# Optimization experiments

Measured on AMD Instinct MI355X. Metric: run time of the kernel, lower is better.

Reference implementation:

```python
import jax, jax.numpy as jnp
import numpy as np

B, D, H, W, Q = 16, 768, 64, 64, 128


def setup_inputs() -> dict:
    key = jax.random.key(0)
    ks = jax.random.split(key, 6)
    s = 0.02  # param init scale
    return {
        "visual_feat": jax.random.normal(ks[0], (B, D, H, W), jnp.float32),
        "text_feat": jax.random.normal(ks[1], (B, Q, D), jnp.float32),
        "Wq": jax.random.normal(ks[2], (D, D), jnp.float32) * s,
        "bq": jnp.zeros((D,), jnp.float32),
        "Wk": jax.random.normal(ks[3], (D, D), jnp.float32) * s,
        "bk": jnp.zeros((D,), jnp.float32),
        "Wv": jax.random.normal(ks[4], (D, D), jnp.float32) * s,
        "bv": jnp.zeros((D,), jnp.float32),
    }


def _entropy_weights(x):
    # x: [B, T, D] -> softmax over features, per-token entropy, softmax over tokens -> [B, T]
    p = jax.nn.softmax(x, axis=-1)
    ent = -jnp.sum(p * jnp.log(p + 1e-9), axis=-1)
    return jax.nn.softmax(ent, axis=-1)


def reference(visual_feat, text_feat, Wq, bq, Wk, bk, Wv, bv):
    b, d, h, w = visual_feat.shape
    vf = visual_feat.reshape(b, d, h * w).transpose(0, 2, 1)  # [B, N, D]
    ve = _entropy_weights(vf)          # [B, N]
    te = _entropy_weights(text_feat)   # [B, Q]
    q = vf @ Wq.T + bq                 # [B, N, D]
    k = text_feat @ Wk.T + bk          # [B, Q, D]
    v = text_feat @ Wv.T + bv          # [B, Q, D]
    attn = jnp.einsum('bnd,bqd->bnq', q, k) / jnp.sqrt(jnp.float32(d))
    attn = attn * (ve[:, :, None] * te[:, None, :])  # entropy outer-product modulation
    attn = jax.nn.softmax(attn, axis=-1)
    enhanced = jnp.einsum('bnq,bqd->bnd', attn, v)   # [B, N, D]
    return enhanced.transpose(0, 2, 1).reshape(b, d, h, w)
```

## Files before the change

kernel.cpp:

```cpp
#include <hip/hip_runtime.h>

#define B_ 16
#define D_ 768
#define N_ 4096
#define Q_ 128

typedef __attribute__((ext_vector_type(4))) float f32x4;
typedef __attribute__((ext_vector_type(8))) short short8;
typedef __attribute__((ext_vector_type(4))) short sv4;

__device__ __forceinline__ unsigned short f2bf(float f) {
  union { float f; unsigned u; } x; x.f = f;
  unsigned u = x.u;
  unsigned r = u + 0x7fffu + ((u >> 16) & 1u);
  return (unsigned short)(r >> 16);
}

__global__ __launch_bounds__(256) void prep_kernel(
    const float* __restrict__ Wv, const float* __restrict__ Wq,
    const float* __restrict__ Wk, const float* __restrict__ bq,
    const float* __restrict__ bk,
    unsigned short* __restrict__ Wvb, unsigned short* __restrict__ WqTb,
    unsigned short* __restrict__ WkTb,
    float* __restrict__ wkbq, float* __restrict__ bias2, float* __restrict__ bqbk) {
  __shared__ float tile[32][33];
  const int z = blockIdx.z;
  const int t = threadIdx.x;
  if (z == 0) {
    int i = (blockIdx.y * 24 + blockIdx.x) * 256 + t;
    float4 v = ((const float4*)Wv)[i];
    ushort4 o;
    o.x = f2bf(v.x); o.y = f2bf(v.y); o.z = f2bf(v.z); o.w = f2bf(v.w);
    ((ushort4*)Wvb)[i] = o;
  } else if (z <= 2) {
    const float* src = (z == 1) ? Wq : Wk;
    unsigned short* dst = (z == 1) ? WqTb : WkTb;
    int bx = blockIdx.x * 32, by = blockIdx.y * 32;
    int tx = t & 31, ty = t >> 5;
    #pragma unroll
    for (int i = 0; i < 32; i += 8)
      tile[ty + i][tx] = src[(size_t)(by + ty + i) * D_ + bx + tx];
    __syncthreads();
    #pragma unroll
    for (int i = 0; i < 32; i += 8)
      dst[(size_t)(bx + ty + i) * D_ + by + tx] = f2bf(tile[tx][ty + i]);
  } else {
    const int bx = blockIdx.x, by = blockIdx.y;
    if (by < 2) {
      if (bx >= 3) return;
      const float* M = by ? Wq : Wk;
      const float* vec = by ? bk : bq;
      float* outp = by ? bias2 : wkbq;
      const int col = bx * 256 + t;
      float s = 0.f;
      #pragma unroll 4
      for (int n = 0; n < D_; n++) s += M[(size_t)n * D_ + col] * vec[n];
      outp[col] = s;
    } else if (by == 2 && bx == 0) {
      float s = 0.f;
      for (int k = t; k < D_; k += 256) s += bq[k] * bk[k];
      #pragma unroll
      for (int off = 32; off; off >>= 1) s += __shfl_xor(s, off);
      __shared__ float red[4];
      if ((t & 63) == 0) red[t >> 6] = s;
      __syncthreads();
      if (t == 0) bqbk[0] = red[0] + red[1] + red[2] + red[3];
    }
  }
}

__global__ __launch_bounds__(256) void entropy_fused_kernel(
    const float* __restrict__ vis, float* __restrict__ ent_v,
    const float* __restrict__ text, unsigned short* __restrict__ textb,
    float* __restrict__ ent_t, const float* __restrict__ wkbq,
    const float* __restrict__ bqbk, float* __restrict__ skq) {
  __shared__ float ss[256], st[256];
  const int t = threadIdx.x;
  if (blockIdx.x < 1024) {
    int bb = blockIdx.x >> 6;
    int n0 = (blockIdx.x & 63) * 64;
    int tok = t & 63, slice = t >> 6;
    const float* base = vis + (size_t)bb * D_ * N_ + (size_t)slice * 192 * N_ + n0 + tok;
    float s = 0.f, tt = 0.f;
    #pragma unroll 4
    for (int d = 0; d < 192; d++) {
      float v = base[(size_t)d * N_];
      float e = __expf(v);
      s += e; tt += v * e;
    }
    ss[t] = s; st[t] = tt;
    __syncthreads();
    if (t < 64) {
      #pragma unroll
      for (int k = 1; k < 4; k++) { s += ss[t + 64 * k]; tt += st[t + 64 * k]; }
      ent_v[(size_t)bb * N_ + n0 + t] = __logf(s) - tt / s;
    }
  } else {
    int row = (blockIdx.x - 1024) * 4 + (t >> 6);
    int lane = t & 63;
    const float4* src = (const float4*)(text + (size_t)row * D_);
    const float4* w4p = (const float4*)wkbq;
    ushort4* dst = (ushort4*)(textb + (size_t)row * D_);
    float s = 0.f, tt = 0.f, s2 = 0.f;
    #pragma unroll
    for (int j = 0; j < 3; j++) {
      float4 v = src[lane + 64 * j];
      float4 w = w4p[lane + 64 * j];
      float e0 = __expf(v.x), e1 = __expf(v.y), e2 = __expf(v.z), e3 = __expf(v.w);
      s += (e0 + e1) + (e2 + e3);
      tt += v.x * e0 + v.y * e1;
      tt += v.z * e2 + v.w * e3;
      s2 += v.x * w.x + v.y * w.y + v.z * w.z + v.w * w.w;
      ushort4 o;
      o.x = f2bf(v.x); o.y = f2bf(v.y); o.z = f2bf(v.z); o.w = f2bf(v.w);
      dst[lane + 64 * j] = o;
    }
    #pragma unroll
    for (int off = 32; off; off >>= 1) {
      s += __shfl_xor(s, off);
      tt += __shfl_xor(tt, off);
      s2 += __shfl_xor(s2, off);
    }
    if (lane == 0) {
      ent_t[row] = __logf(s) - tt / s;
      skq[row] = s2 + bqbk[0];
    }
  }
}

__global__ __launch_bounds__(1024) void softmax_fused_kernel(
    const float* __restrict__ ent_v, float* __restrict__ vew,
    const float* __restrict__ ent_t, float* __restrict__ tew) {
  __shared__ float red[32];
  __shared__ float sv[128];
  const int b = blockIdx.x, t = threadIdx.x;
  if (b < 16) {
    const float* e = ent_v + (size_t)b * N_;
    float v[4];
    float m = -__builtin_inff();
    #pragma unroll
    for (int i = 0; i < 4; i++) { v[i] = e[t + 1024 * i]; m = fmaxf(m, v[i]); }
    #pragma unroll
    for (int off = 32; off; off >>= 1) m = fmaxf(m, __shfl_xor(m, off));
    int wv = t >> 6;
    if ((t & 63) == 0) red[wv] = m;
    __syncthreads();
    if (t < 16) {
      float x = red[t];
      #pragma unroll
      for (int off = 8; off; off >>= 1) x = fmaxf(x, __shfl_xor(x, off));
      red[t] = x;
    }
    __syncthreads();
    m = red[0];
    float ev[4];
    float s = 0.f;
    #pragma unroll
    for (int i = 0; i < 4; i++) { ev[i] = __expf(v[i] - m); s += ev[i]; }
    #pragma unroll
    for (int off = 32; off; off >>= 1) s += __shfl_xor(s, off);
    __syncthreads();
    if ((t & 63) == 0) red[wv] = s;
    __syncthreads();
    if (t < 16) {
      float x = red[t];
      #pragma unroll
      for (int off = 8; off; off >>= 1) x += __shfl_xor(x, off);
      red[t] = x;
    }
    __syncthreads();
    s = red[0];
    #pragma unroll
    for (int i = 0; i < 4; i++) vew[(size_t)b * N_ + t + 1024 * i] = ev[i] / s;
  } else {
    const int bb = b - 16;
    float v = 0.f;
    if (t < 128) { v = ent_t[bb * 128 + t]; sv[t] = v; }
    __syncthreads();
    if (t < 64) {
      float m = fmaxf(sv[t], sv[t + 64]);
      #pragma unroll
      for (int off = 32; off; off >>= 1) m = fmaxf(m, __shfl_xor(m, off));
      if (t == 0) red[0] = m;
    }
    __syncthreads();
    const float m = red[0];
    float e = 0.f;
    if (t < 128) { e = __expf(v - m); sv[t] = e; }
    __syncthreads();
    if (t < 64) {
      float s = sv[t] + sv[t + 64];
      #pragma unroll
      for (int off = 32; off; off >>= 1) s += __shfl_xor(s, off);
      if (t == 0) red[1] = s;
    }
    __syncthreads();
    if (t < 128) tew[bb * 128 + t] = e / red[1];
  }
}

__global__ __launch_bounds__(256) void gemm_nt_kernel(
    const unsigned short* __restrict__ A, const unsigned short* __restrict__ Bm,
    unsigned short* __restrict__ C) {
  constexpr int LDA = 72;
  __shared__ unsigned short As[64 * LDA];
  __shared__ unsigned short Bs[64 * LDA];
  int m0 = blockIdx.x * 64, n0 = blockIdx.y * 64;
  int t = threadIdx.x, wave = t >> 6, lane = t & 63;
  int wm = (wave & 1) * 32, wn = (wave >> 1) * 32;
  int fl = lane & 15, fq = lane >> 4;
  f32x4 acc[2][2];
  #pragma unroll
  for (int i = 0; i < 2; i++)
    #pragma unroll
    for (int j = 0; j < 2; j++) acc[i][j] = {0.f, 0.f, 0.f, 0.f};
  for (int k0 = 0; k0 < D_; k0 += 64) {
    __syncthreads();
    #pragma unroll
    for (int i = 0; i < 2; i++) {
      int c = t + 256 * i;
      int sr = c >> 3, sc = (c & 7) * 8;
      *(uint4*)(As + sr * LDA + sc) = *(const uint4*)(A + (size_t)(m0 + sr) * D_ + k0 + sc);
      *(uint4*)(Bs + sr * LDA + sc) = *(const uint4*)(Bm + (size_t)(n0 + sr) * D_ + k0 + sc);
    }
    __syncthreads();
    #pragma unroll
    for (int ks = 0; ks < 2; ks++) {
      short8 afr[2], bfr[2];
      #pragma unroll
      for (int i = 0; i < 2; i++)
        afr[i] = *(const short8*)(As + (wm + i * 16 + fl) * LDA + ks * 32 + fq * 8);
      #pragma unroll
      for (int j = 0; j < 2; j++)
        bfr[j] = *(const short8*)(Bs + (wn + j * 16 + fl) * LDA + ks * 32 + fq * 8);
      #pragma unroll
      for (int i = 0; i < 2; i++)
        #pragma unroll
        for (int j = 0; j < 2; j++)
          acc[i][j] = __builtin_amdgcn_mfma_f32_16x16x32_bf16(afr[i], bfr[j], acc[i][j], 0, 0, 0);
    }
  }
  #pragma unroll
  for (int i = 0; i < 2; i++)
    #pragma unroll
    for (int j = 0; j < 2; j++) {
      int n = n0 + wn + j * 16 + fl;
      #pragma unroll
      for (int r = 0; r < 4; r++) {
        int m = m0 + wm + i * 16 + fq * 4 + r;
        C[(size_t)m * D_ + n] = f2bf(acc[i][j][r]);
      }
    }
}

__global__ __launch_bounds__(256) void gemm_kqvT_kernel(
    const unsigned short* __restrict__ A, const unsigned short* __restrict__ W2T,
    const float* __restrict__ bias2, unsigned short* __restrict__ kqb,
    const unsigned short* __restrict__ Wvb, const float* __restrict__ bv,
    unsigned short* __restrict__ vTb) {
  constexpr int LDA = 72;
  __shared__ unsigned short As[64 * LDA];
  __shared__ unsigned short Bs[64 * LDA];
  const bool isV = blockIdx.y >= 12;
  const unsigned short* Bm = isV ? Wvb : W2T;
  const float* bias = isV ? bv : bias2;
  unsigned short* C = isV ? vTb : kqb;
  int m0 = blockIdx.x * 64, n0 = (isV ? blockIdx.y - 12 : blockIdx.y) * 64;
  int t = threadIdx.x, wave = t >> 6, lane = t & 63;
  int wm = (wave & 1) * 32, wn = (wave >> 1) * 32;
  int fl = lane & 15, fq = lane >> 4;
  f32x4 acc[2][2];
  #pragma unroll
  for (int i = 0; i < 2; i++)
    #pragma unroll
    for (int j = 0; j < 2; j++) acc[i][j] = {0.f, 0.f, 0.f, 0.f};
  for (int k0 = 0; k0 < D_; k0 += 64) {
    __syncthreads();
    #pragma unroll
    for (int i = 0; i < 2; i++) {
      int c = t + 256 * i;
      int sr = c >> 3, sc = (c & 7) * 8;
      *(uint4*)(As + sr * LDA + sc) = *(const uint4*)(A + (size_t)(m0 + sr) * D_ + k0 + sc);
      *(uint4*)(Bs + sr * LDA + sc) = *(const uint4*)(Bm + (size_t)(n0 + sr) * D_ + k0 + sc);
    }
    __syncthreads();
    #pragma unroll
    for (int ks = 0; ks < 2; ks++) {
      short8 afr[2], bfr[2];
      #pragma unroll
      for (int i = 0; i < 2; i++)
        afr[i] = *(const short8*)(As + (wm + i * 16 + fl) * LDA + ks * 32 + fq * 8);
      #pragma unroll
      for (int j = 0; j < 2; j++)
        bfr[j] = *(const short8*)(Bs + (wn + j * 16 + fl) * LDA + ks * 32 + fq * 8);
      #pragma unroll
      for (int i = 0; i < 2; i++)
        #pragma unroll
        for (int j = 0; j < 2; j++)
          acc[i][j] = __builtin_amdgcn_mfma_f32_16x16x32_bf16(afr[i], bfr[j], acc[i][j], 0, 0, 0);
    }
  }
  #pragma unroll
  for (int i = 0; i < 2; i++)
    #pragma unroll
    for (int j = 0; j < 2; j++) {
      int n = n0 + wn + j * 16 + fl;
      float bb = bias[n];
      #pragma unroll
      for (int r = 0; r < 4; r++) {
        int m = m0 + wm + i * 16 + fq * 4 + r;
        float val = acc[i][j][r] + bb;
        if (isV) {
          int bt = m >> 7, q = m & 127;
          C[((size_t)bt * D_ + n) * Q_ + q] = f2bf(val);
        } else {
          C[(size_t)m * D_ + n] = f2bf(val);
        }
      }
    }
}

__global__ __launch_bounds__(256, 2) void attn_main_kernel(
    const float* __restrict__ vis,
    const unsigned short* __restrict__ kq,
    const unsigned short* __restrict__ vT,
    const float* __restrict__ ve,
    const float* __restrict__ te,
    const float* __restrict__ skq,
    float* __restrict__ out)
{
  constexpr int LA = 68;
  constexpr int LB = 72;
  constexpr int LP = 136;
  __shared__ unsigned short region0[30464];
  __shared__ float stats[2][128][2];
  unsigned short* As = region0;
  unsigned short* Bs = region0 + 8704;
  unsigned short* Ps = region0;
  unsigned short* Vs = region0 + 17408;

  const int bb = blockIdx.x >> 5;
  const int n0 = (blockIdx.x & 31) * 128;
  const int t = threadIdx.x;
  const int wave = t >> 6, lane = t & 63;
  const int fl = lane & 15, fq = lane >> 4;
  const int wm = (wave & 1) * 64;
  const int wq = (wave >> 1) * 64;

  const float* abase = vis + (size_t)bb * D_ * N_ + n0;
  const unsigned short* bbase = kq + (size_t)bb * Q_ * D_;

  f32x4 acc[4][4];
  #pragma unroll
  for (int i = 0; i < 4; i++)
    #pragma unroll
    for (int j = 0; j < 4; j++) acc[i][j] = {0.f, 0.f, 0.f, 0.f};

  const int smi = t & 127;
  const int ph = t >> 7;

  for (int k0 = 0; k0 < D_; k0 += 64) {
    __syncthreads();
    #pragma unroll
    for (int i = 0; i < 16; i++) {
      const int kk = 2 * (ph + 2 * i);
      const float v0 = abase[(size_t)(k0 + kk) * N_ + smi];
      const float v1 = abase[(size_t)(k0 + kk + 1) * N_ + smi];
      const unsigned pk = (unsigned)f2bf(v0) | ((unsigned)f2bf(v1) << 16);
      *(unsigned*)(As + smi * LA + kk) = pk;
    }
    #pragma unroll
    for (int i = 0; i < 4; i++) {
      const int c = t + 256 * i;
      const int q = c >> 3, kc = (c & 7) * 8;
      const uint4 v = *(const uint4*)(bbase + (size_t)q * D_ + k0 + kc);
      *(uint4*)(Bs + q * LB + kc) = v;
    }
    __syncthreads();
    #pragma unroll
    for (int ks = 0; ks < 2; ks++) {
      short8 afr[4], bfr[4];
      #pragma unroll
      for (int i = 0; i < 4; i++) {
        const unsigned short* pa = As + (wm + i * 16 + fl) * LA + ks * 32 + fq * 8;
        sv4 lo = *(const sv4*)pa;
        sv4 hi = *(const sv4*)(pa + 4);
        afr[i] = __builtin_shufflevector(lo, hi, 0, 1, 2, 3, 4, 5, 6, 7);
      }
      #pragma unroll
      for (int j = 0; j < 4; j++)
        bfr[j] = *(const short8*)(Bs + (wq + j * 16 + fl) * LB + ks * 32 + fq * 8);
      #pragma unroll
      for (int i = 0; i < 4; i++)
        #pragma unroll
        for (int j = 0; j < 4; j++)
          acc[i][j] = __builtin_amdgcn_mfma_f32_16x16x32_bf16(afr[i], bfr[j], acc[i][j], 0, 0, 0);
    }
  }

  const float rsD = 0.03608439182435161f;
  float tev[4], skv[4];
  #pragma unroll
  for (int j = 0; j < 4; j++) {
    int q = wq + j * 16 + fl;
    tev[j] = te[bb * Q_ + q];
    skv[j] = skq[bb * Q_ + q];
  }
  float vev4[4][4];
  #pragma unroll
  for (int i = 0; i < 4; i++)
    #pragma unroll
    for (int r = 0; r < 4; r++)
      vev4[i][r] = ve[(size_t)bb * N_ + n0 + wm + i * 16 + fq * 4 + r];

  float rmax[4][4], rsum[4][4];
  #pragma unroll
  for (int i = 0; i < 4; i++)
    #pragma unroll
    for (int r = 0; r < 4; r++) rmax[i][r] = -__builtin_inff();
  #pragma unroll
  for (int i = 0; i < 4; i++)
    #pragma unroll
    for (int j = 0; j < 4; j++)
      #pragma unroll
      for (int r = 0; r < 4; r++) {
        float L = (acc[i][j][r] + skv[j]) * rsD * vev4[i][r] * tev[j];
        acc[i][j][r] = L;
        rmax[i][r] = fmaxf(rmax[i][r], L);
      }
  #pragma unroll
  for (int off = 1; off < 16; off <<= 1)
    #pragma unroll
    for (int i = 0; i < 4; i++)
      #pragma unroll
      for (int r = 0; r < 4; r++)
        rmax[i][r] = fmaxf(rmax[i][r], __shfl_xor(rmax[i][r], off));
  #pragma unroll
  for (int i = 0; i < 4; i++)
    #pragma unroll
    for (int r = 0; r < 4; r++) rsum[i][r] = 0.f;
  #pragma unroll
  for (int i = 0; i < 4; i++)
    #pragma unroll
    for (int j = 0; j < 4; j++)
      #pragma unroll
      for (int r = 0; r < 4; r++) {
        float e = __expf(acc[i][j][r] - rmax[i][r]);
        acc[i][j][r] = e;
        rsum[i][r] += e;
      }
  #pragma unroll
  for (int off = 1; off < 16; off <<= 1)
    #pragma unroll
    for (int i = 0; i < 4; i++)
      #pragma unroll
      for (int r = 0; r < 4; r++) rsum[i][r] += __shfl_xor(rsum[i][r], off);

  const int qh = wq >> 6;
  if (fl == 0) {
    #pragma unroll
    for (int i = 0; i < 4; i++)
      #pragma unroll
      for (int r = 0; r < 4; r++) {
        int m = wm + i * 16 + fq * 4 + r;
        stats[qh][m][0] = rmax[i][r];
        stats[qh][m][1] = rsum[i][r];
      }
  }
  __syncthreads();
  float fac[4][4];
  #pragma unroll
  for (int i = 0; i < 4; i++)
    #pragma unroll
    for (int r = 0; r < 4; r++) {
      int m = wm + i * 16 + fq * 4 + r;
      float M2 = stats[1 - qh][m][0], S2 = stats[1 - qh][m][1];
      float Mf = fmaxf(rmax[i][r], M2);
      float sf = rsum[i][r] * __expf(rmax[i][r] - Mf) + S2 * __expf(M2 - Mf);
      fac[i][r] = __expf(rmax[i][r] - Mf) / sf;
    }
  #pragma unroll
  for (int i = 0; i < 4; i++)
    #pragma unroll
    for (int j = 0; j < 4; j++)
      #pragma unroll
      for (int r = 0; r < 4; r++) {
        int m = wm + i * 16 + fq * 4 + r;
        int q = wq + j * 16 + fl;
        Ps[m * LP + q] = f2bf(acc[i][j][r] * fac[i][r]);
      }

  const int wd = (wave & 1) * 48;
  const int wm2 = (wave >> 1) * 64;
  for (int dc = 0; dc < 8; dc++) {
    __syncthreads();
    const unsigned short* vbase = vT + ((size_t)bb * D_ + dc * 96) * Q_;
    #pragma unroll
    for (int i = 0; i < 6; i++) {
      const int c = t + 256 * i;
      const int d = c >> 4, qc = (c & 15) * 8;
      const uint4 v = *(const uint4*)(vbase + (size_t)d * Q_ + qc);
      *(uint4*)(Vs + d * LP + qc) = v;
    }
    __syncthreads();
    f32x4 acc2[3][4];
    #pragma unroll
    for (int i = 0; i < 3; i++)
      #pragma unroll
      for (int j = 0; j < 4; j++) acc2[i][j] = {0.f, 0.f, 0.f, 0.f};
    #pragma unroll
    for (int ks = 0; ks < 4; ks++) {
      short8 vfr[3], pfr[4];
      #pragma unroll
      for (int i = 0; i < 3; i++)
        vfr[i] = *(const short8*)(Vs + (wd + i * 16 + fl) * LP + ks * 32 + fq * 8);
      #pragma unroll
      for (int j = 0; j < 4; j++)
        pfr[j] = *(const short8*)(Ps + (wm2 + j * 16 + fl) * LP + ks * 32 + fq * 8);
      #pragma unroll
      for (int i = 0; i < 3; i++)
        #pragma unroll
        for (int j = 0; j < 4; j++)
          acc2[i][j] = __builtin_amdgcn_mfma_f32_16x16x32_bf16(vfr[i], pfr[j], acc2[i][j], 0, 0, 0);
    }
    float* obase = out + ((size_t)bb * D_ + dc * 96) * N_ + n0;
    #pragma unroll
    for (int i = 0; i < 3; i++)
      #pragma unroll
      for (int j = 0; j < 4; j++) {
        int mm = wm2 + j * 16 + fl;
        #pragma unroll
        for (int r = 0; r < 4; r++) {
          int d = wd + i * 16 + fq * 4 + r;
          obase[(size_t)d * N_ + mm] = acc2[i][j][r];
        }
      }
  }
}

extern "C" void kernel_launch(void* const* d_in, const int* in_sizes, int n_in,
                              void* d_out, int out_size, void* d_ws, size_t ws_size,
                              hipStream_t stream) {
  const float* vis  = (const float*)d_in[0];
  const float* text = (const float*)d_in[1];
  const float* Wq   = (const float*)d_in[2];
  const float* bq   = (const float*)d_in[3];
  const float* Wk   = (const float*)d_in[4];
  const float* bk   = (const float*)d_in[5];
  const float* Wv   = (const float*)d_in[6];
  const float* bv   = (const float*)d_in[7];
  float* out = (float*)d_out;
  char* ws = (char*)d_ws;

  unsigned short* textb = (unsigned short*)(ws + 0);
  unsigned short* WkTb  = (unsigned short*)(ws + 3145728);
  unsigned short* Wvb   = (unsigned short*)(ws + 4325376);
  unsigned short* WqTb  = (unsigned short*)(ws + 5505024);
  unsigned short* W2Tb  = (unsigned short*)(ws + 6684672);
  float* wkbq  = (float*)(ws + 7864320);
  float* bias2 = (float*)(ws + 7867392);
  float* bqbk  = (float*)(ws + 7870464);
  unsigned short* kqb   = (unsigned short*)(ws + 9830400);
  unsigned short* vTb   = (unsigned short*)(ws + 12976128);
  float* ent_t = (float*)(ws + 16121856);
  float* tew   = (float*)(ws + 16130048);
  float* ent_v = (float*)(ws + 16138240);
  float* vew   = (float*)(ws + 16400384);
  float* skq   = (float*)(ws + 16662528);

  prep_kernel<<<dim3(24, 24, 4), 256, 0, stream>>>(Wv, Wq, Wk, bq, bk,
                                                   Wvb, WqTb, WkTb, wkbq, bias2, bqbk);
  entropy_fused_kernel<<<1536, 256, 0, stream>>>(vis, ent_v, text, textb, ent_t,
                                                 wkbq, bqbk, skq);
  softmax_fused_kernel<<<32, 1024, 0, stream>>>(ent_v, vew, ent_t, tew);
  gemm_nt_kernel<<<dim3(12, 12), 256, 0, stream>>>(WqTb, WkTb, W2Tb);
  gemm_kqvT_kernel<<<dim3(32, 24), 256, 0, stream>>>(textb, W2Tb, bias2, kqb, Wvb, bv, vTb);
  attn_main_kernel<<<512, 256, 0, stream>>>(vis, kqb, vTb, vew, tew, skq, out);
}
```

Baseline: 507.6 us.

## Fuse visual entropy into score GEMM and split attention into two kernels

New measurement: 634.7 us. 25.0% more time.

```diff
diff --git a/kernel.cpp b/kernel.cpp
--- a/kernel.cpp
+++ b/kernel.cpp
@@ -69,62 +69,38 @@
   }
 }
 
-__global__ __launch_bounds__(256) void entropy_fused_kernel(
-    const float* __restrict__ vis, float* __restrict__ ent_v,
+__global__ __launch_bounds__(256) void text_prep_kernel(
     const float* __restrict__ text, unsigned short* __restrict__ textb,
     float* __restrict__ ent_t, const float* __restrict__ wkbq,
     const float* __restrict__ bqbk, float* __restrict__ skq) {
-  __shared__ float ss[256], st[256];
-  const int t = threadIdx.x;
-  if (blockIdx.x < 1024) {
-    int bb = blockIdx.x >> 6;
-    int n0 = (blockIdx.x & 63) * 64;
-    int tok = t & 63, slice = t >> 6;
-    const float* base = vis + (size_t)bb * D_ * N_ + (size_t)slice * 192 * N_ + n0 + tok;
-    float s = 0.f, tt = 0.f;
-    #pragma unroll 4
-    for (int d = 0; d < 192; d++) {
-      float v = base[(size_t)d * N_];
-      float e = __expf(v);
-      s += e; tt += v * e;
-    }
-    ss[t] = s; st[t] = tt;
-    __syncthreads();
-    if (t < 64) {
-      #pragma unroll
-      for (int k = 1; k < 4; k++) { s += ss[t + 64 * k]; tt += st[t + 64 * k]; }
-      ent_v[(size_t)bb * N_ + n0 + t] = __logf(s) - tt / s;
-    }
-  } else {
-    int row = (blockIdx.x - 1024) * 4 + (t >> 6);
-    int lane = t & 63;
-    const float4* src = (const float4*)(text + (size_t)row * D_);
-    const float4* w4p = (const float4*)wkbq;
-    ushort4* dst = (ushort4*)(textb + (size_t)row * D_);
-    float s = 0.f, tt = 0.f, s2 = 0.f;
-    #pragma unroll
-    for (int j = 0; j < 3; j++) {
-      float4 v = src[lane + 64 * j];
-      float4 w = w4p[lane + 64 * j];
-      float e0 = __expf(v.x), e1 = __expf(v.y), e2 = __expf(v.z), e3 = __expf(v.w);
-      s += (e0 + e1) + (e2 + e3);
-      tt += v.x * e0 + v.y * e1;
-      tt += v.z * e2 + v.w * e3;
-      s2 += v.x * w.x + v.y * w.y + v.z * w.z + v.w * w.w;
-      ushort4 o;
-      o.x = f2bf(v.x); o.y = f2bf(v.y); o.z = f2bf(v.z); o.w = f2bf(v.w);
-      dst[lane + 64 * j] = o;
-    }
-    #pragma unroll
-    for (int off = 32; off; off >>= 1) {
-      s += __shfl_xor(s, off);
-      tt += __shfl_xor(tt, off);
-      s2 += __shfl_xor(s2, off);
-    }
-    if (lane == 0) {
-      ent_t[row] = __logf(s) - tt / s;
-      skq[row] = s2 + bqbk[0];
-    }
+  int row = blockIdx.x * 4 + (threadIdx.x >> 6);
+  int lane = threadIdx.x & 63;
+  const float4* src = (const float4*)(text + (size_t)row * D_);
+  const float4* w4p = (const float4*)wkbq;
+  ushort4* dst = (ushort4*)(textb + (size_t)row * D_);
+  float s = 0.f, tt = 0.f, s2 = 0.f;
+  #pragma unroll
+  for (int j = 0; j < 3; j++) {
+    float4 v = src[lane + 64 * j];
+    float4 w = w4p[lane + 64 * j];
+    float e0 = __expf(v.x), e1 = __expf(v.y), e2 = __expf(v.z), e3 = __expf(v.w);
+    s += (e0 + e1) + (e2 + e3);
+    tt += v.x * e0 + v.y * e1;
+    tt += v.z * e2 + v.w * e3;
+    s2 += v.x * w.x + v.y * w.y + v.z * w.z + v.w * w.w;
+    ushort4 o;
+    o.x = f2bf(v.x); o.y = f2bf(v.y); o.z = f2bf(v.z); o.w = f2bf(v.w);
+    dst[lane + 64 * j] = o;
+  }
+  #pragma unroll
+  for (int off = 32; off; off >>= 1) {
+    s += __shfl_xor(s, off);
+    tt += __shfl_xor(tt, off);
+    s2 += __shfl_xor(s2, off);
+  }
+  if (lane == 0) {
+    ent_t[row] = __logf(s) - tt / s;
+    skq[row] = s2 + bqbk[0];
   }
 }
 
@@ -320,24 +296,17 @@
     }
 }
 
-__global__ __launch_bounds__(256, 2) void attn_main_kernel(
+__global__ __launch_bounds__(256, 4) void attn_s_kernel(
     const float* __restrict__ vis,
     const unsigned short* __restrict__ kq,
-    const unsigned short* __restrict__ vT,
-    const float* __restrict__ ve,
-    const float* __restrict__ te,
-    const float* __restrict__ skq,
-    float* __restrict__ out)
+    float* __restrict__ S,
+    float* __restrict__ ent_v)
 {
   constexpr int LA = 68;
   constexpr int LB = 72;
-  constexpr int LP = 136;
-  __shared__ unsigned short region0[30464];
-  __shared__ float stats[2][128][2];
-  unsigned short* As = region0;
-  unsigned short* Bs = region0 + 8704;
-  unsigned short* Ps = region0;
-  unsigned short* Vs = region0 + 17408;
+  __shared__ unsigned short As[128 * LA];
+  __shared__ unsigned short Bs[128 * LB];
+  __shared__ float esh[512];
 
   const int bb = blockIdx.x >> 5;
   const int n0 = (blockIdx.x & 31) * 128;
@@ -358,6 +327,7 @@
 
   const int smi = t & 127;
   const int ph = t >> 7;
+  float es = 0.f, ets = 0.f;
 
   for (int k0 = 0; k0 < D_; k0 += 64) {
     __syncthreads();
@@ -366,6 +336,9 @@
       const int kk = 2 * (ph + 2 * i);
       const float v0 = abase[(size_t)(k0 + kk) * N_ + smi];
       const float v1 = abase[(size_t)(k0 + kk + 1) * N_ + smi];
+      const float e0 = __expf(v0), e1 = __expf(v1);
+      es += e0 + e1;
+      ets += v0 * e0 + v1 * e1;
       const unsigned pk = (unsigned)f2bf(v0) | ((unsigned)f2bf(v1) << 16);
       *(unsigned*)(As + smi * LA + kk) = pk;
     }
@@ -398,6 +371,57 @@
     }
   }
 
+  esh[t] = es;
+  esh[256 + t] = ets;
+  __syncthreads();
+  if (t < 128) {
+    const float Sx = es + esh[t + 128];
+    const float Tx = ets + esh[384 + t];
+    ent_v[(size_t)bb * N_ + n0 + t] = __logf(Sx) - Tx / Sx;
+  }
+
+  float* sbase = S + ((size_t)bb * N_ + n0) * Q_;
+  #pragma unroll
+  for (int i = 0; i < 4; i++)
+    #pragma unroll
+    for (int j = 0; j < 4; j++)
+      #pragma unroll
+      for (int r = 0; r < 4; r++)
+        sbase[(size_t)(wm + i * 16 + fq * 4 + r) * Q_ + wq + j * 16 + fl] = acc[i][j][r];
+}
+
+__global__ __launch_bounds__(256, 3) void attn_pv_kernel(
+    const float* __restrict__ S,
+    const unsigned short* __restrict__ vT,
+    const float* __restrict__ ve,
+    const float* __restrict__ te,
+    const float* __restrict__ skq,
+    float* __restrict__ out)
+{
+  constexpr int LP = 136;
+  __shared__ unsigned short region0[26112];
+  unsigned short* Ps = region0;
+  unsigned short* Vs = region0 + 17408;
+  float* stats = (float*)(region0 + 17408);
+
+  const int bb = blockIdx.x >> 5;
+  const int n0 = (blockIdx.x & 31) * 128;
+  const int t = threadIdx.x;
+  const int wave = t >> 6, lane = t & 63;
+  const int fl = lane & 15, fq = lane >> 4;
+  const int wm = (wave & 1) * 64;
+  const int wq = (wave >> 1) * 64;
+
+  f32x4 acc[4][4];
+  const float* sbase = S + ((size_t)bb * N_ + n0) * Q_;
+  #pragma unroll
+  for (int i = 0; i < 4; i++)
+    #pragma unroll
+    for (int j = 0; j < 4; j++)
+      #pragma unroll
+      for (int r = 0; r < 4; r++)
+        acc[i][j][r] = sbase[(size_t)(wm + i * 16 + fq * 4 + r) * Q_ + wq + j * 16 + fl];
+
   const float rsD = 0.03608439182435161f;
   float tev[4], skv[4];
   #pragma unroll
@@ -463,8 +487,8 @@
       #pragma unroll
       for (int r = 0; r < 4; r++) {
         int m = wm + i * 16 + fq * 4 + r;
-        stats[qh][m][0] = rmax[i][r];
-        stats[qh][m][1] = rsum[i][r];
+        stats[(qh * 128 + m) * 2 + 0] = rmax[i][r];
+        stats[(qh * 128 + m) * 2 + 1] = rsum[i][r];
       }
   }
   __syncthreads();
@@ -474,7 +498,8 @@
     #pragma unroll
     for (int r = 0; r < 4; r++) {
       int m = wm + i * 16 + fq * 4 + r;
-      float M2 = stats[1 - qh][m][0], S2 = stats[1 - qh][m][1];
+      float M2 = stats[((1 - qh) * 128 + m) * 2 + 0];
+      float S2 = stats[((1 - qh) * 128 + m) * 2 + 1];
       float Mf = fmaxf(rmax[i][r], M2);
       float sf = rsum[i][r] * __expf(rmax[i][r] - Mf) + S2 * __expf(M2 - Mf);
       fac[i][r] = __expf(rmax[i][r] - Mf) / sf;
@@ -490,42 +515,41 @@
         Ps[m * LP + q] = f2bf(acc[i][j][r] * fac[i][r]);
       }
 
-  const int wd = (wave & 1) * 48;
+  const int wd = (wave & 1) * 32;
   const int wm2 = (wave >> 1) * 64;
-  for (int dc = 0; dc < 8; dc++) {
-    __syncthreads();
-    const unsigned short* vbase = vT + ((size_t)bb * D_ + dc * 96) * Q_;
-    #pragma unroll
-    for (int i = 0; i < 6; i++) {
+  for (int dc = 0; dc < 12; dc++) {
+    __syncthreads();
+    const unsigned short* vbase = vT + ((size_t)bb * D_ + dc * 64) * Q_;
+    #pragma unroll
+    for (int i = 0; i < 4; i++) {
       const int c = t + 256 * i;
       const int d = c >> 4, qc = (c & 15) * 8;
-      const uint4 v = *(const uint4*)(vbase + (size_t)d * Q_ + qc);
-      *(uint4*)(Vs + d * LP + qc) = v;
-    }
-    __syncthreads();
-    f32x4 acc2[3][4];
-    #pragma unroll
-    for (int i = 0; i < 3; i++)
+      *(uint4*)(Vs + d * LP + qc) = *(const uint4*)(vbase + (size_t)d * Q_ + qc);
+    }
+    __syncthreads();
+    f32x4 acc2[2][4];
+    #pragma unroll
+    for (int i = 0; i < 2; i++)
       #pragma unroll
       for (int j = 0; j < 4; j++) acc2[i][j] = {0.f, 0.f, 0.f, 0.f};
     #pragma unroll
     for (int ks = 0; ks < 4; ks++) {
-      short8 vfr[3], pfr[4];
-      #pragma unroll
-      for (int i = 0; i < 3; i++)
+      short8 vfr[2], pfr[4];
+      #pragma unroll
+      for (int i = 0; i < 2; i++)
         vfr[i] = *(const short8*)(Vs + (wd + i * 16 + fl) * LP + ks * 32 + fq * 8);
       #pragma unroll
       for (int j = 0; j < 4; j++)
         pfr[j] = *(const short8*)(Ps + (wm2 + j * 16 + fl) * LP + ks * 32 + fq * 8);
       #pragma unroll
-      for (int i = 0; i < 3; i++)
+      for (int i = 0; i < 2; i++)
         #pragma unroll
         for (int j = 0; j < 4; j++)
           acc2[i][j] = __builtin_amdgcn_mfma_f32_16x16x32_bf16(vfr[i], pfr[j], acc2[i][j], 0, 0, 0);
     }
-    float* obase = out + ((size_t)bb * D_ + dc * 96) * N_ + n0;
-    #pragma unroll
-    for (int i = 0; i < 3; i++)
+    float* obase = out + ((size_t)bb * D_ + dc * 64) * N_ + n0;
+    #pragma unroll
+    for (int i = 0; i < 2; i++)
       #pragma unroll
       for (int j = 0; j < 4; j++) {
         int mm = wm2 + j * 16 + fl;
@@ -567,13 +591,14 @@
   float* ent_v = (float*)(ws + 16138240);
   float* vew   = (float*)(ws + 16400384);
   float* skq   = (float*)(ws + 16662528);
+  float* Sbuf  = (float*)(ws + 16777216);
 
   prep_kernel<<<dim3(24, 24, 4), 256, 0, stream>>>(Wv, Wq, Wk, bq, bk,
                                                    Wvb, WqTb, WkTb, wkbq, bias2, bqbk);
-  entropy_fused_kernel<<<1536, 256, 0, stream>>>(vis, ent_v, text, textb, ent_t,
-                                                 wkbq, bqbk, skq);
-  softmax_fused_kernel<<<32, 1024, 0, stream>>>(ent_v, vew, ent_t, tew);
+  text_prep_kernel<<<512, 256, 0, stream>>>(text, textb, ent_t, wkbq, bqbk, skq);
   gemm_nt_kernel<<<dim3(12, 12), 256, 0, stream>>>(WqTb, WkTb, W2Tb);
   gemm_kqvT_kernel<<<dim3(32, 24), 256, 0, stream>>>(textb, W2Tb, bias2, kqb, Wvb, bv, vTb);
-  attn_main_kernel<<<512, 256, 0, stream>>>(vis, kqb, vTb, vew, tew, skq, out);
-}
+  attn_s_kernel<<<512, 256, 0, stream>>>(vis, kqb, Sbuf, ent_v);
+  softmax_fused_kernel<<<32, 1024, 0, stream>>>(ent_v, vew, ent_t, tew);
+  attn_pv_kernel<<<512, 256, 0, stream>>>(Sbuf, vTb, vew, tew, skq, out);
+}
```
